# Optimization experiments

Hardware: AMD Instinct MI355X
Metric: run time of the kernel (lower is better)

## Reference

```python
import jax, jax.numpy as jnp
import numpy as np

LN_EPS = 1e-5

def _conv1d(x, w, b):
    # x: [B, T, Cin], w: [Cout, Cin, K] (torch layout), pad=1 -> same length for K=3
    y = jax.lax.conv_general_dilated(
        x, jnp.transpose(w, (2, 1, 0)), window_strides=(1,), padding=[(1, 1)],
        dimension_numbers=('NWC', 'WIO', 'NWC'))
    return y + b

def _layernorm(x, g, b):
    mu = jnp.mean(x, axis=-1, keepdims=True)
    var = jnp.mean(jnp.square(x - mu), axis=-1, keepdims=True)
    return (x - mu) * jax.lax.rsqrt(var + LN_EPS) * g + b

def _duration_predictor(enc, mask, w1, b1, g1, beta1, w2, b2, g2, beta2, wl, bl):
    x = enc * mask                                  # [B,T,C]
    x = _layernorm(jax.nn.relu(_conv1d(x, w1, b1)), g1, beta1)
    x = _layernorm(jax.nn.relu(_conv1d(x, w2, b2)), g2, beta2)
    out = x @ wl.T + bl                             # [B,T,1]
    return (out * mask)[..., 0]                     # [B,T]

def _expand_one(enc_i, dur_i, M):
    # enc_i: [T,C], dur_i: [T] int; fused repeat_interleave via searchsorted gather
    cs = jnp.cumsum(dur_i)                          # [T]
    pos = jnp.arange(M)                             # [M]
    idx = jnp.searchsorted(cs, pos, side='right')   # token index for each frame
    valid = pos < cs[-1]
    out = jnp.where(valid[:, None], enc_i[jnp.clip(idx, 0, enc_i.shape[0] - 1)], 0.0)
    dec = jnp.where(valid, pos + 1, 0)
    return out, dec

def setup_inputs() -> dict:
    key = jax.random.key(0)
    ks = jax.random.split(key, 12)
    B, T, C, F, M = 32, 512, 384, 384, 2048
    s = lambda n: 1.0 / np.sqrt(n)
    return {
        'encoder_output': jax.random.normal(ks[0], (B, T, C), jnp.float32),
        'encoder_output_mask': jnp.ones((B, T, 1), jnp.float32),
        'target': jax.random.randint(ks[1], (B, T), 0, 8, jnp.int32),
        'mel_max_length': M,
        'w1': jax.random.normal(ks[2], (F, C, 3), jnp.float32) * s(C * 3),
        'b1': jnp.zeros((F,), jnp.float32),
        'g1': jnp.ones((F,), jnp.float32),
        'beta1': jnp.zeros((F,), jnp.float32),
        'w2': jax.random.normal(ks[3], (F, F, 3), jnp.float32) * s(F * 3),
        'b2': jnp.zeros((F,), jnp.float32),
        'g2': jnp.ones((F,), jnp.float32),
        'beta2': jnp.zeros((F,), jnp.float32),
        'wl': jax.random.normal(ks[4], (1, F), jnp.float32) * s(F),
        'bl': jnp.zeros((1,), jnp.float32),
    }

def reference(encoder_output, encoder_output_mask, target, mel_max_length,
              w1, b1, g1, beta1, w2, b2, g2, beta2, wl, bl):
    # training-mode forward: durations come from `target`, alpha=1.0
    dpo = _duration_predictor(encoder_output, encoder_output_mask,
                              w1, b1, g1, beta1, w2, b2, g2, beta2, wl, bl)
    repeats = jnp.round(target.astype(jnp.float32) * 1.0).astype(jnp.int32)
    output, dec_pos = jax.vmap(lambda e, d: _expand_one(e, d, mel_max_length))(
        encoder_output, repeats)
    return output, dec_pos, dpo
```

## Files before the change

### kernel.cpp

```cpp
#include <hip/hip_runtime.h>
#include <hip/hip_bf16.h>
#include <stdint.h>

#define B_ 32
#define T_ 512
#define C_ 384
#define F_ 384
#define M_ 2048
#define PT (T_ + 2)
#define KTOT (3 * C_)

typedef __bf16 bf16x8 __attribute__((ext_vector_type(8)));
typedef float  f32x4  __attribute__((ext_vector_type(4)));
typedef unsigned short ushort_t;

__device__ __forceinline__ ushort_t f2bf(float f) {
  __hip_bfloat16 h = __float2bfloat16(f);
  return *reinterpret_cast<ushort_t*>(&h);
}
__device__ __forceinline__ uint32_t pack2(float a, float b) {
  return (uint32_t)f2bf(a) | ((uint32_t)f2bf(b) << 16);
}

#define NWB 3456
__global__ __launch_bounds__(256) void prep_kernel(
    const int* __restrict__ target,
    const float* __restrict__ w1, const float* __restrict__ w2,
    ushort_t* __restrict__ x1p,
    ushort_t* __restrict__ wt1, ushort_t* __restrict__ wt2,
    int* __restrict__ cs) {
  const int gid = blockIdx.x;
  const int tid = threadIdx.x;
  if (gid < NWB) {
    int idx = gid * 256 + tid;
    int w = idx >= F_ * KTOT;
    int o = idx - (w ? F_ * KTOT : 0);
    int n = o / KTOT, k = o - n * KTOT;
    int kk = k / C_, c = k - kk * C_;
    int s = kk * 6 + (c >> 6);
    int c64 = c & 63;
    int ks = c64 >> 5, qq = (c64 >> 3) & 3, e = c64 & 7;
    int wv = n / 48, rn = n - wv * 48, fn = rn >> 4, r16 = rn & 15;
    int lane = qq * 16 + r16;
    size_t dst = ((((size_t)s * 8 + wv) * 6 + fn * 2 + ks) << 9) + lane * 8 + e;
    const float* src = w ? w2 : w1;
    (w ? wt2 : wt1)[dst] = f2bf(src[(n * C_ + c) * 3 + kk]);
  } else if (gid < NWB + 48) {
    int idx = (gid - NWB) * 256 + tid;
    int bb = idx / C_, c = idx - bb * C_;
    x1p[(size_t)(bb * PT) * C_ + c] = 0;
    x1p[(size_t)(bb * PT + T_ + 1) * C_ + c] = 0;
  } else {
    int b = (gid - NWB - 48) * 4 + (tid >> 6);
    int lane = tid & 63;
    int base = b * T_ + lane * 8;
    int v[8];
#pragma unroll
    for (int i = 0; i < 8; ++i) v[i] = target[base + i];
#pragma unroll
    for (int i = 1; i < 8; ++i) v[i] += v[i - 1];
    int tot = v[7];
    int inc = tot;
#pragma unroll
    for (int d = 1; d < 64; d <<= 1) {
      int t = __shfl_up(inc, d);
      if (lane >= d) inc += t;
    }
    int excl = inc - tot;
#pragma unroll
    for (int i = 0; i < 8; ++i) cs[base + i] = v[i] + excl;
  }
}

template <bool LAST>
__global__ __launch_bounds__(512, 1) void gemm_ln_kernel(
    const float* __restrict__ enc,
    const float* __restrict__ mask,
    const ushort_t* __restrict__ x1p,
    const ushort_t* __restrict__ wt,
    const float* __restrict__ bias, const float* __restrict__ g,
    const float* __restrict__ be,
    const float* __restrict__ wl, const float* __restrict__ bl,
    ushort_t* __restrict__ xout,
    float* __restrict__ dpo) {
  __shared__ char ldsX[66 * 768];
  __shared__ float red[8][64][2];
  __shared__ float stats[64][2];

  const int tid = threadIdx.x;
  const int l = tid & 63, q = l >> 4, r16 = l & 15;
  const int wid = tid >> 6;
  const int b = blockIdx.x >> 3, t0 = (blockIdx.x & 7) * 64;

  if (!LAST) {
#pragma unroll
    for (int ps = 0; ps < 7; ++ps) {
      int idx = ps * 512 + tid;
      if (idx < 66 * 48) {
        int rl = idx / 48, cp = idx - rl * 48;
        int gc = cp >> 3, ch = cp & 7;
        int t = t0 - 1 + rl;
        uint4 o = make_uint4(0, 0, 0, 0);
        if (t >= 0 && t < T_) {
          const float* src = enc + ((size_t)b * T_ + t) * C_ + gc * 64 + ch * 8;
          float4 u = *(const float4*)src;
          float4 v = *(const float4*)(src + 4);
          float m = mask[b * T_ + t];
          o = make_uint4(pack2(u.x * m, u.y * m), pack2(u.z * m, u.w * m),
                         pack2(v.x * m, v.y * m), pack2(v.z * m, v.w * m));
        }
        *(uint4*)(ldsX + rl * 768 + gc * 128 + ((ch ^ (rl & 7)) << 4)) = o;
      }
    }
  } else {
#pragma unroll
    for (int ps = 0; ps < 7; ++ps) {
      int idx = ps * 512 + tid;
      if (idx < 66 * 48) {
        int rl = idx / 48, cp = idx - rl * 48;
        int gc = cp >> 3, ch = cp & 7;
        uint4 v = *(const uint4*)(x1p + ((size_t)(b * PT + t0 + rl)) * C_ +
                                  gc * 64 + ch * 8);
        *(uint4*)(ldsX + rl * 768 + gc * 128 + ((ch ^ (rl & 7)) << 4)) = v;
      }
    }
  }

  f32x4 acc[3][4];
#pragma unroll
  for (int fn = 0; fn < 3; ++fn)
#pragma unroll
    for (int fm = 0; fm < 4; ++fm) acc[fn][fm] = (f32x4){0.f, 0.f, 0.f, 0.f};

  const ushort_t* wlane = wt + ((size_t)wid * 6 << 9) + (l << 3);
  auto LOADW = [&](bf16x8 (&dst)[3][2], int s) {
    const ushort_t* p = wlane + (((size_t)s * 8 * 6) << 9);
#pragma unroll
    for (int fn = 0; fn < 3; ++fn)
#pragma unroll
      for (int ks = 0; ks < 2; ++ks)
        dst[fn][ks] = *(const bf16x8*)(p + ((fn * 2 + ks) << 9));
  };
  auto COMP = [&](bf16x8 (&af)[3][2], int s) {
    const int kk = s / 6, c128 = (s % 6) * 128;
#pragma unroll
    for (int ks = 0; ks < 2; ++ks) {
      bf16x8 bx[4];
#pragma unroll
      for (int fm = 0; fm < 4; ++fm) {
        int rl = fm * 16 + r16 + kk;
        bx[fm] = *(const bf16x8*)(ldsX + rl * 768 + c128 +
                                  (((ks * 4 + q) ^ (rl & 7)) << 4));
      }
#pragma unroll
      for (int fn = 0; fn < 3; ++fn)
#pragma unroll
        for (int fm = 0; fm < 4; ++fm)
          acc[fn][fm] = __builtin_amdgcn_mfma_f32_16x16x32_bf16(
              af[fn][ks], bx[fm], acc[fn][fm], 0, 0, 0);
    }
  };

  bf16x8 afA[3][2], afB[3][2];
  LOADW(afA, 0);
  __syncthreads();
#pragma unroll 1
  for (int s = 0; s < 18; s += 2) {
    LOADW(afB, s + 1);
    COMP(afA, s);
    if (s + 2 < 18) LOADW(afA, s + 2);
    COMP(afB, s + 1);
  }

#pragma unroll
  for (int fn = 0; fn < 3; ++fn) {
    const int nb = wid * 48 + fn * 16 + q * 4;
    float b0 = bias[nb], b1 = bias[nb + 1], b2 = bias[nb + 2], b3 = bias[nb + 3];
#pragma unroll
    for (int fm = 0; fm < 4; ++fm) {
      acc[fn][fm][0] = fmaxf(acc[fn][fm][0] + b0, 0.f);
      acc[fn][fm][1] = fmaxf(acc[fn][fm][1] + b1, 0.f);
      acc[fn][fm][2] = fmaxf(acc[fn][fm][2] + b2, 0.f);
      acc[fn][fm][3] = fmaxf(acc[fn][fm][3] + b3, 0.f);
    }
  }

#pragma unroll
  for (int fm = 0; fm < 4; ++fm) {
    float s = 0.f, s2 = 0.f;
#pragma unroll
    for (int fn = 0; fn < 3; ++fn)
#pragma unroll
      for (int j = 0; j < 4; ++j) {
        float v = acc[fn][fm][j];
        s += v; s2 += v * v;
      }
    s += __shfl_xor(s, 16); s += __shfl_xor(s, 32);
    s2 += __shfl_xor(s2, 16); s2 += __shfl_xor(s2, 32);
    if (l < 16) { red[wid][fm * 16 + r16][0] = s; red[wid][fm * 16 + r16][1] = s2; }
  }
  __syncthreads();
  if (tid < 64) {
    float S = 0.f, S2 = 0.f;
#pragma unroll
    for (int w = 0; w < 8; ++w) { S += red[w][tid][0]; S2 += red[w][tid][1]; }
    float mu = S / F_;
    stats[tid][0] = mu;
    stats[tid][1] = rsqrtf(S2 / F_ - mu * mu + 1e-5f);
  }
  __syncthreads();

  if (!LAST) {
#pragma unroll
    for (int fn = 0; fn < 3; ++fn) {
      const int nb = wid * 48 + fn * 16 + q * 4;
      float g0 = g[nb], g1 = g[nb + 1], g2 = g[nb + 2], g3 = g[nb + 3];
      float e0 = be[nb], e1 = be[nb + 1], e2 = be[nb + 2], e3 = be[nb + 3];
#pragma unroll
      for (int fm = 0; fm < 4; ++fm) {
        const int m = fm * 16 + r16;
        const float mu = stats[m][0], rs = stats[m][1];
        uint32_t p0 = pack2((acc[fn][fm][0] - mu) * rs * g0 + e0,
                            (acc[fn][fm][1] - mu) * rs * g1 + e1);
        uint32_t p1 = pack2((acc[fn][fm][2] - mu) * rs * g2 + e2,
                            (acc[fn][fm][3] - mu) * rs * g3 + e3);
        *(uint2*)(xout + ((size_t)(b * PT + 1 + t0 + m)) * C_ + nb) =
            make_uint2(p0, p1);
      }
    }
  } else {
    float p[4] = {0.f, 0.f, 0.f, 0.f};
#pragma unroll
    for (int fn = 0; fn < 3; ++fn) {
      const int nb = wid * 48 + fn * 16 + q * 4;
      float g0 = g[nb], g1 = g[nb + 1], g2 = g[nb + 2], g3 = g[nb + 3];
      float e0 = be[nb], e1 = be[nb + 1], e2 = be[nb + 2], e3 = be[nb + 3];
      float l0 = wl[nb], l1 = wl[nb + 1], l2 = wl[nb + 2], l3 = wl[nb + 3];
#pragma unroll
      for (int fm = 0; fm < 4; ++fm) {
        const int m = fm * 16 + r16;
        const float mu = stats[m][0], rs = stats[m][1];
        p[fm] += ((acc[fn][fm][0] - mu) * rs * g0 + e0) * l0 +
                 ((acc[fn][fm][1] - mu) * rs * g1 + e1) * l1 +
                 ((acc[fn][fm][2] - mu) * rs * g2 + e2) * l2 +
                 ((acc[fn][fm][3] - mu) * rs * g3 + e3) * l3;
      }
    }
    __syncthreads();
#pragma unroll
    for (int fm = 0; fm < 4; ++fm) {
      float s = p[fm];
      s += __shfl_xor(s, 16); s += __shfl_xor(s, 32);
      if (l < 16) red[wid][fm * 16 + r16][0] = s;
    }
    __syncthreads();
    if (tid < 64) {
      float S = 0.f;
#pragma unroll
      for (int w = 0; w < 8; ++w) S += red[w][tid][0];
      int t = t0 + tid;
      dpo[b * T_ + t] = (S + bl[0]) * mask[b * T_ + t];
    }
  }
}

__global__ __launch_bounds__(256) void expand_kernel(
    const float* __restrict__ enc,
    const int* __restrict__ cs,
    float* __restrict__ out,
    float* __restrict__ dec) {
  __shared__ int scs[T_];
  const int blk = blockIdx.x;
  const int b = blk / (M_ / 4);
  const int p0 = (blk - b * (M_ / 4)) * 4;
  for (int i = threadIdx.x; i < T_; i += 256) scs[i] = cs[b * T_ + i];
  __syncthreads();

  const int lane = threadIdx.x & 63;
  const int wid = threadIdx.x >> 6;
  const int pos = p0 + wid;
  const int total = scs[T_ - 1];
  const bool valid = pos < total;

  int idx = 0;
#pragma unroll
  for (int step = 512; step; step >>= 1)
    if (idx + step <= T_ && scs[idx + step - 1] <= pos) idx += step;
  int src = idx < T_ ? idx : T_ - 1;

  const float4* srow = (const float4*)(enc + ((size_t)b * T_ + src) * C_);
  float4* orow = (float4*)(out + ((size_t)b * M_ + pos) * C_);
  const float4 zero = make_float4(0.f, 0.f, 0.f, 0.f);
#pragma unroll
  for (int j = 0; j < 2; ++j) {
    int c4 = j * 64 + lane;
    if (c4 < C_ / 4) orow[c4] = valid ? srow[c4] : zero;
  }
  if (lane == 0) dec[b * M_ + pos] = valid ? (float)(pos + 1) : 0.f;
}

extern "C" void kernel_launch(void* const* d_in, const int* in_sizes, int n_in,
                              void* d_out, int out_size, void* d_ws,
                              size_t ws_size, hipStream_t stream) {
  const float* enc    = (const float*)d_in[0];
  const float* mask   = (const float*)d_in[1];
  const int*   target = (const int*)d_in[2];
  const float* w1    = (const float*)d_in[4];
  const float* b1    = (const float*)d_in[5];
  const float* g1    = (const float*)d_in[6];
  const float* beta1 = (const float*)d_in[7];
  const float* w2    = (const float*)d_in[8];
  const float* b2    = (const float*)d_in[9];
  const float* g2    = (const float*)d_in[10];
  const float* beta2 = (const float*)d_in[11];
  const float* wl    = (const float*)d_in[12];
  const float* bl    = (const float*)d_in[13];

  ushort_t* x1p = (ushort_t*)d_ws;
  ushort_t* wt1 = x1p + (size_t)B_ * PT * C_;
  ushort_t* wt2 = wt1 + (size_t)F_ * KTOT;
  int*      cs  = (int*)(wt2 + (size_t)F_ * KTOT);

  float* out0 = (float*)d_out;
  float* dec  = out0 + (size_t)B_ * M_ * C_;
  float* dpo  = dec + (size_t)B_ * M_;

  prep_kernel<<<NWB + 48 + 8, 256, 0, stream>>>(
      target, w1, w2, x1p, wt1, wt2, cs);

  gemm_ln_kernel<false><<<B_ * (T_ / 64), 512, 0, stream>>>(
      enc, mask, nullptr, wt1, b1, g1, beta1, nullptr, nullptr, x1p, nullptr);
  gemm_ln_kernel<true><<<B_ * (T_ / 64), 512, 0, stream>>>(
      nullptr, mask, x1p, wt2, b2, g2, beta2, wl, bl, nullptr, dpo);

  expand_kernel<<<(B_ * M_) / 4, 256, 0, stream>>>(enc, cs, out0, dec);
}
```

Before: 80.93 us.

## Fuse expand work into GEMM-LN launches as extra heterogeneous blocks

Drops the separate expand kernel and splits its gather-copy work into two halves, each handled by 256 extra blocks appended to the two conv GEMM+LayerNorm launches. The memory-bound expand copy can then run on CUs alongside the compute-bound GEMM blocks, which also removes one launch. Launch bounds are raised to two blocks per CU, and the weight double-buffer prefetch is restructured to load both stages inside each loop iteration. This lowers register pressure but weakens the overlap of weight loads with MFMA work.

New measurement: 111.5 us. +37.8%, slower.

```diff
diff --git a/kernel.cpp b/kernel.cpp
--- a/kernel.cpp
+++ b/kernel.cpp
@@ -72,17 +72,20 @@
   }
 }
 
-template <bool LAST>
-__global__ __launch_bounds__(512, 1) void gemm_ln_kernel(
+template <int PART>
+__global__ __launch_bounds__(512, 2) void hetero_kernel(
     const float* __restrict__ enc,
     const float* __restrict__ mask,
-    const ushort_t* __restrict__ x1p,
+    const ushort_t* __restrict__ x1p_in,
+    ushort_t* __restrict__ x1p_out,
     const ushort_t* __restrict__ wt,
     const float* __restrict__ bias, const float* __restrict__ g,
     const float* __restrict__ be,
     const float* __restrict__ wl, const float* __restrict__ bl,
-    ushort_t* __restrict__ xout,
-    float* __restrict__ dpo) {
+    float* __restrict__ dpo,
+    const int* __restrict__ cs,
+    float* __restrict__ out0,
+    float* __restrict__ dec) {
   __shared__ char ldsX[66 * 768];
   __shared__ float red[8][64][2];
   __shared__ float stats[64][2];
@@ -90,9 +93,37 @@
   const int tid = threadIdx.x;
   const int l = tid & 63, q = l >> 4, r16 = l & 15;
   const int wid = tid >> 6;
+
+  if (blockIdx.x >= 256) {
+    const int eb = blockIdx.x - 256;
+    const int b = eb >> 3;
+    const int p0 = (eb & 7) * 128 + PART * (M_ / 2);
+    int* scs = (int*)ldsX;
+    for (int i = tid; i < T_; i += 512) scs[i] = cs[b * T_ + i];
+    __syncthreads();
+    const int total = scs[T_ - 1];
+    const float4 zero = make_float4(0.f, 0.f, 0.f, 0.f);
+#pragma unroll 1
+    for (int it = 0; it < 16; ++it) {
+      const int pos = p0 + it * 8 + wid;
+      const bool valid = pos < total;
+      int idx = 0;
+#pragma unroll
+      for (int step = 512; step; step >>= 1)
+        if (idx + step <= T_ && scs[idx + step - 1] <= pos) idx += step;
+      int src = idx < T_ ? idx : T_ - 1;
+      const float4* srow = (const float4*)(enc + ((size_t)b * T_ + src) * C_);
+      float4* orow = (float4*)(out0 + ((size_t)b * M_ + pos) * C_);
+      orow[l] = valid ? srow[l] : zero;
+      if (l < 32) orow[64 + l] = valid ? srow[64 + l] : zero;
+      if (l == 0) dec[b * M_ + pos] = valid ? (float)(pos + 1) : 0.f;
+    }
+    return;
+  }
+
   const int b = blockIdx.x >> 3, t0 = (blockIdx.x & 7) * 64;
 
-  if (!LAST) {
+  if (PART == 0) {
 #pragma unroll
     for (int ps = 0; ps < 7; ++ps) {
       int idx = ps * 512 + tid;
@@ -119,7 +150,7 @@
       if (idx < 66 * 48) {
         int rl = idx / 48, cp = idx - rl * 48;
         int gc = cp >> 3, ch = cp & 7;
-        uint4 v = *(const uint4*)(x1p + ((size_t)(b * PT + t0 + rl)) * C_ +
+        uint4 v = *(const uint4*)(x1p_in + ((size_t)(b * PT + t0 + rl)) * C_ +
                                   gc * 64 + ch * 8);
         *(uint4*)(ldsX + rl * 768 + gc * 128 + ((ch ^ (rl & 7)) << 4)) = v;
       }
@@ -161,14 +192,13 @@
     }
   };
 
-  bf16x8 afA[3][2], afB[3][2];
-  LOADW(afA, 0);
   __syncthreads();
 #pragma unroll 1
   for (int s = 0; s < 18; s += 2) {
+    bf16x8 afA[3][2], afB[3][2];
+    LOADW(afA, s);
     LOADW(afB, s + 1);
     COMP(afA, s);
-    if (s + 2 < 18) LOADW(afA, s + 2);
     COMP(afB, s + 1);
   }
 
@@ -210,7 +240,7 @@
   }
   __syncthreads();
 
-  if (!LAST) {
+  if (PART == 0) {
 #pragma unroll
     for (int fn = 0; fn < 3; ++fn) {
       const int nb = wid * 48 + fn * 16 + q * 4;
@@ -224,7 +254,7 @@
                             (acc[fn][fm][1] - mu) * rs * g1 + e1);
         uint32_t p1 = pack2((acc[fn][fm][2] - mu) * rs * g2 + e2,
                             (acc[fn][fm][3] - mu) * rs * g3 + e3);
-        *(uint2*)(xout + ((size_t)(b * PT + 1 + t0 + m)) * C_ + nb) =
+        *(uint2*)(x1p_out + ((size_t)(b * PT + 1 + t0 + m)) * C_ + nb) =
             make_uint2(p0, p1);
       }
     }
@@ -262,41 +292,6 @@
       dpo[b * T_ + t] = (S + bl[0]) * mask[b * T_ + t];
     }
   }
-}
-
-__global__ __launch_bounds__(256) void expand_kernel(
-    const float* __restrict__ enc,
-    const int* __restrict__ cs,
-    float* __restrict__ out,
-    float* __restrict__ dec) {
-  __shared__ int scs[T_];
-  const int blk = blockIdx.x;
-  const int b = blk / (M_ / 4);
-  const int p0 = (blk - b * (M_ / 4)) * 4;
-  for (int i = threadIdx.x; i < T_; i += 256) scs[i] = cs[b * T_ + i];
-  __syncthreads();
-
-  const int lane = threadIdx.x & 63;
-  const int wid = threadIdx.x >> 6;
-  const int pos = p0 + wid;
-  const int total = scs[T_ - 1];
-  const bool valid = pos < total;
-
-  int idx = 0;
-#pragma unroll
-  for (int step = 512; step; step >>= 1)
-    if (idx + step <= T_ && scs[idx + step - 1] <= pos) idx += step;
-  int src = idx < T_ ? idx : T_ - 1;
-
-  const float4* srow = (const float4*)(enc + ((size_t)b * T_ + src) * C_);
-  float4* orow = (float4*)(out + ((size_t)b * M_ + pos) * C_);
-  const float4 zero = make_float4(0.f, 0.f, 0.f, 0.f);
-#pragma unroll
-  for (int j = 0; j < 2; ++j) {
-    int c4 = j * 64 + lane;
-    if (c4 < C_ / 4) orow[c4] = valid ? srow[c4] : zero;
-  }
-  if (lane == 0) dec[b * M_ + pos] = valid ? (float)(pos + 1) : 0.f;
 }
 
 extern "C" void kernel_launch(void* const* d_in, const int* in_sizes, int n_in,
@@ -328,10 +323,10 @@
   prep_kernel<<<NWB + 48 + 8, 256, 0, stream>>>(
       target, w1, w2, x1p, wt1, wt2, cs);
 
-  gemm_ln_kernel<false><<<B_ * (T_ / 64), 512, 0, stream>>>(
-      enc, mask, nullptr, wt1, b1, g1, beta1, nullptr, nullptr, x1p, nullptr);
-  gemm_ln_kernel<true><<<B_ * (T_ / 64), 512, 0, stream>>>(
-      nullptr, mask, x1p, wt2, b2, g2, beta2, wl, bl, nullptr, dpo);
-
-  expand_kernel<<<(B_ * M_) / 4, 256, 0, stream>>>(enc, cs, out0, dec);
-}
+  hetero_kernel<0><<<512, 512, 0, stream>>>(
+      enc, mask, nullptr, x1p, wt1, b1, g1, beta1, nullptr, nullptr,
+      nullptr, cs, out0, dec);
+  hetero_kernel<1><<<512, 512, 0, stream>>>(
+      enc, mask, x1p, nullptr, wt2, b2, g2, beta2, wl, bl,
+      dpo, cs, out0, dec);
+}
```

## Fuse both conv+LayerNorm stages into one kernel using halo recompute

Applied to the files above, without the earlier changes.

Merges the two conv-GEMM+LayerNorm kernels into a single kernel. Each block loads a 2-row halo of input, computes conv1 over 80 rows (66 used) and writes the normalized bf16 result into LDS, then runs conv2 directly from LDS. This removes the global round trip of the intermediate activation, the padding-zero pass in the prep kernel, and one launch. The cost is about 25% extra conv1 MFMA work from the halo recompute, more accumulator registers and a larger LDS footprint.

Result: faster. 75.97 us (-6.1%).

```diff
diff --git a/kernel.cpp b/kernel.cpp
--- a/kernel.cpp
+++ b/kernel.cpp
@@ -7,7 +7,6 @@
 #define C_ 384
 #define F_ 384
 #define M_ 2048
-#define PT (T_ + 2)
 #define KTOT (3 * C_)
 
 typedef __bf16 bf16x8 __attribute__((ext_vector_type(8)));
@@ -26,7 +25,6 @@
 __global__ __launch_bounds__(256) void prep_kernel(
     const int* __restrict__ target,
     const float* __restrict__ w1, const float* __restrict__ w2,
-    ushort_t* __restrict__ x1p,
     ushort_t* __restrict__ wt1, ushort_t* __restrict__ wt2,
     int* __restrict__ cs) {
   const int gid = blockIdx.x;
@@ -45,13 +43,8 @@
     size_t dst = ((((size_t)s * 8 + wv) * 6 + fn * 2 + ks) << 9) + lane * 8 + e;
     const float* src = w ? w2 : w1;
     (w ? wt2 : wt1)[dst] = f2bf(src[(n * C_ + c) * 3 + kk]);
-  } else if (gid < NWB + 48) {
-    int idx = (gid - NWB) * 256 + tid;
-    int bb = idx / C_, c = idx - bb * C_;
-    x1p[(size_t)(bb * PT) * C_ + c] = 0;
-    x1p[(size_t)(bb * PT + T_ + 1) * C_ + c] = 0;
   } else {
-    int b = (gid - NWB - 48) * 4 + (tid >> 6);
+    int b = (gid - NWB) * 4 + (tid >> 6);
     int lane = tid & 63;
     int base = b * T_ + lane * 8;
     int v[8];
@@ -72,76 +65,163 @@
   }
 }
 
-template <bool LAST>
-__global__ __launch_bounds__(512, 1) void gemm_ln_kernel(
+__global__ __launch_bounds__(512, 1) void gemm12_kernel(
     const float* __restrict__ enc,
     const float* __restrict__ mask,
-    const ushort_t* __restrict__ x1p,
-    const ushort_t* __restrict__ wt,
-    const float* __restrict__ bias, const float* __restrict__ g,
-    const float* __restrict__ be,
+    const ushort_t* __restrict__ wt1,
+    const ushort_t* __restrict__ wt2,
+    const float* __restrict__ b1, const float* __restrict__ g1,
+    const float* __restrict__ be1,
+    const float* __restrict__ b2, const float* __restrict__ g2,
+    const float* __restrict__ be2,
     const float* __restrict__ wl, const float* __restrict__ bl,
-    ushort_t* __restrict__ xout,
     float* __restrict__ dpo) {
-  __shared__ char ldsX[66 * 768];
-  __shared__ float red[8][64][2];
-  __shared__ float stats[64][2];
+  __shared__ char ldsX[82 * 768];
+  __shared__ float red[8][80][2];
+  __shared__ float stats[80][2];
 
   const int tid = threadIdx.x;
   const int l = tid & 63, q = l >> 4, r16 = l & 15;
   const int wid = tid >> 6;
   const int b = blockIdx.x >> 3, t0 = (blockIdx.x & 7) * 64;
 
-  if (!LAST) {
-#pragma unroll
-    for (int ps = 0; ps < 7; ++ps) {
-      int idx = ps * 512 + tid;
-      if (idx < 66 * 48) {
-        int rl = idx / 48, cp = idx - rl * 48;
-        int gc = cp >> 3, ch = cp & 7;
-        int t = t0 - 1 + rl;
-        uint4 o = make_uint4(0, 0, 0, 0);
-        if (t >= 0 && t < T_) {
-          const float* src = enc + ((size_t)b * T_ + t) * C_ + gc * 64 + ch * 8;
-          float4 u = *(const float4*)src;
-          float4 v = *(const float4*)(src + 4);
-          float m = mask[b * T_ + t];
-          o = make_uint4(pack2(u.x * m, u.y * m), pack2(u.z * m, u.w * m),
-                         pack2(v.x * m, v.y * m), pack2(v.z * m, v.w * m));
-        }
-        *(uint4*)(ldsX + rl * 768 + gc * 128 + ((ch ^ (rl & 7)) << 4)) = o;
-      }
-    }
-  } else {
-#pragma unroll
-    for (int ps = 0; ps < 7; ++ps) {
-      int idx = ps * 512 + tid;
-      if (idx < 66 * 48) {
-        int rl = idx / 48, cp = idx - rl * 48;
-        int gc = cp >> 3, ch = cp & 7;
-        uint4 v = *(const uint4*)(x1p + ((size_t)(b * PT + t0 + rl)) * C_ +
-                                  gc * 64 + ch * 8);
-        *(uint4*)(ldsX + rl * 768 + gc * 128 + ((ch ^ (rl & 7)) << 4)) = v;
-      }
-    }
-  }
-
-  f32x4 acc[3][4];
+#pragma unroll
+  for (int ps = 0; ps < 8; ++ps) {
+    int idx = ps * 512 + tid;
+    if (idx < 82 * 48) {
+      int rl = idx / 48, cp = idx - rl * 48;
+      int gc = cp >> 3, ch = cp & 7;
+      int t = t0 - 2 + rl;
+      uint4 o = make_uint4(0, 0, 0, 0);
+      if (t >= 0 && t < T_) {
+        const float* src = enc + ((size_t)b * T_ + t) * C_ + gc * 64 + ch * 8;
+        float4 u = *(const float4*)src;
+        float4 v = *(const float4*)(src + 4);
+        float m = mask[b * T_ + t];
+        o = make_uint4(pack2(u.x * m, u.y * m), pack2(u.z * m, u.w * m),
+                       pack2(v.x * m, v.y * m), pack2(v.z * m, v.w * m));
+      }
+      *(uint4*)(ldsX + rl * 768 + gc * 128 + ((ch ^ (rl & 7)) << 4)) = o;
+    }
+  }
+
+  f32x4 acc1[3][5];
 #pragma unroll
   for (int fn = 0; fn < 3; ++fn)
 #pragma unroll
-    for (int fm = 0; fm < 4; ++fm) acc[fn][fm] = (f32x4){0.f, 0.f, 0.f, 0.f};
-
-  const ushort_t* wlane = wt + ((size_t)wid * 6 << 9) + (l << 3);
-  auto LOADW = [&](bf16x8 (&dst)[3][2], int s) {
-    const ushort_t* p = wlane + (((size_t)s * 8 * 6) << 9);
+    for (int fm = 0; fm < 5; ++fm) acc1[fn][fm] = (f32x4){0.f, 0.f, 0.f, 0.f};
+
+  const ushort_t* wlane1 = wt1 + ((size_t)wid * 6 << 9) + (l << 3);
+  const ushort_t* wlane2 = wt2 + ((size_t)wid * 6 << 9) + (l << 3);
+  auto LOADW = [&](const ushort_t* wlane, bf16x8 (&dst)[3][2], int s) {
+    const ushort_t* p = wlane + (((size_t)s * 48) << 9);
 #pragma unroll
     for (int fn = 0; fn < 3; ++fn)
 #pragma unroll
       for (int ks = 0; ks < 2; ++ks)
         dst[fn][ks] = *(const bf16x8*)(p + ((fn * 2 + ks) << 9));
   };
-  auto COMP = [&](bf16x8 (&af)[3][2], int s) {
+  auto COMP1 = [&](bf16x8 (&af)[3][2], int s) {
+    const int kk = s / 6, c128 = (s % 6) * 128;
+#pragma unroll
+    for (int ks = 0; ks < 2; ++ks) {
+      bf16x8 bx[5];
+#pragma unroll
+      for (int fm = 0; fm < 5; ++fm) {
+        int rl = fm * 16 + r16 + kk;
+        bx[fm] = *(const bf16x8*)(ldsX + rl * 768 + c128 +
+                                  (((ks * 4 + q) ^ (rl & 7)) << 4));
+      }
+#pragma unroll
+      for (int fn = 0; fn < 3; ++fn)
+#pragma unroll
+        for (int fm = 0; fm < 5; ++fm)
+          acc1[fn][fm] = __builtin_amdgcn_mfma_f32_16x16x32_bf16(
+              af[fn][ks], bx[fm], acc1[fn][fm], 0, 0, 0);
+    }
+  };
+
+  {
+    bf16x8 afA[3][2], afB[3][2];
+    LOADW(wlane1, afA, 0);
+    __syncthreads();
+#pragma unroll 1
+    for (int s = 0; s < 18; s += 2) {
+      LOADW(wlane1, afB, s + 1);
+      COMP1(afA, s);
+      if (s + 2 < 18) LOADW(wlane1, afA, s + 2);
+      COMP1(afB, s + 1);
+    }
+  }
+
+#pragma unroll
+  for (int fn = 0; fn < 3; ++fn) {
+    const int nb = wid * 48 + fn * 16 + q * 4;
+    float c0 = b1[nb], c1 = b1[nb + 1], c2 = b1[nb + 2], c3 = b1[nb + 3];
+#pragma unroll
+    for (int fm = 0; fm < 5; ++fm) {
+      acc1[fn][fm][0] = fmaxf(acc1[fn][fm][0] + c0, 0.f);
+      acc1[fn][fm][1] = fmaxf(acc1[fn][fm][1] + c1, 0.f);
+      acc1[fn][fm][2] = fmaxf(acc1[fn][fm][2] + c2, 0.f);
+      acc1[fn][fm][3] = fmaxf(acc1[fn][fm][3] + c3, 0.f);
+    }
+  }
+#pragma unroll
+  for (int fm = 0; fm < 5; ++fm) {
+    float s = 0.f, s2 = 0.f;
+#pragma unroll
+    for (int fn = 0; fn < 3; ++fn)
+#pragma unroll
+      for (int j = 0; j < 4; ++j) {
+        float v = acc1[fn][fm][j];
+        s += v; s2 += v * v;
+      }
+    s += __shfl_xor(s, 16); s += __shfl_xor(s, 32);
+    s2 += __shfl_xor(s2, 16); s2 += __shfl_xor(s2, 32);
+    if (l < 16) { red[wid][fm * 16 + r16][0] = s; red[wid][fm * 16 + r16][1] = s2; }
+  }
+  __syncthreads();
+  if (tid < 66) {
+    float S = 0.f, S2 = 0.f;
+#pragma unroll
+    for (int w = 0; w < 8; ++w) { S += red[w][tid][0]; S2 += red[w][tid][1]; }
+    float mu = S / F_;
+    stats[tid][0] = mu;
+    stats[tid][1] = rsqrtf(S2 / F_ - mu * mu + 1e-5f);
+  }
+  __syncthreads();
+
+#pragma unroll
+  for (int fn = 0; fn < 3; ++fn) {
+    const int nb = wid * 48 + fn * 16 + q * 4;
+    float g0 = g1[nb], gg1 = g1[nb + 1], g2v = g1[nb + 2], g3 = g1[nb + 3];
+    float e0 = be1[nb], e1 = be1[nb + 1], e2 = be1[nb + 2], e3 = be1[nb + 3];
+#pragma unroll
+    for (int fm = 0; fm < 5; ++fm) {
+      const int m = fm * 16 + r16;
+      if (m < 66) {
+        const float mu = stats[m][0], rs = stats[m][1];
+        uint32_t p0 = pack2((acc1[fn][fm][0] - mu) * rs * g0 + e0,
+                            (acc1[fn][fm][1] - mu) * rs * gg1 + e1);
+        uint32_t p1 = pack2((acc1[fn][fm][2] - mu) * rs * g2v + e2,
+                            (acc1[fn][fm][3] - mu) * rs * g3 + e3);
+        *(uint2*)(ldsX + m * 768 + (((nb >> 3) ^ (m & 7)) << 4) +
+                  ((q & 1) << 3)) = make_uint2(p0, p1);
+      }
+    }
+  }
+  if (t0 == 0 && tid < 48)
+    *(uint4*)(ldsX + tid * 16) = make_uint4(0, 0, 0, 0);
+  if (t0 == T_ - 64 && tid < 48)
+    *(uint4*)(ldsX + 65 * 768 + tid * 16) = make_uint4(0, 0, 0, 0);
+
+  f32x4 acc2[3][4];
+#pragma unroll
+  for (int fn = 0; fn < 3; ++fn)
+#pragma unroll
+    for (int fm = 0; fm < 4; ++fm) acc2[fn][fm] = (f32x4){0.f, 0.f, 0.f, 0.f};
+
+  auto COMP2 = [&](bf16x8 (&af)[3][2], int s) {
     const int kk = s / 6, c128 = (s % 6) * 128;
 #pragma unroll
     for (int ks = 0; ks < 2; ++ks) {
@@ -156,35 +236,37 @@
       for (int fn = 0; fn < 3; ++fn)
 #pragma unroll
         for (int fm = 0; fm < 4; ++fm)
-          acc[fn][fm] = __builtin_amdgcn_mfma_f32_16x16x32_bf16(
-              af[fn][ks], bx[fm], acc[fn][fm], 0, 0, 0);
+          acc2[fn][fm] = __builtin_amdgcn_mfma_f32_16x16x32_bf16(
+              af[fn][ks], bx[fm], acc2[fn][fm], 0, 0, 0);
     }
   };
 
-  bf16x8 afA[3][2], afB[3][2];
-  LOADW(afA, 0);
-  __syncthreads();
+  {
+    bf16x8 afA[3][2], afB[3][2];
+    LOADW(wlane2, afA, 0);
+    __syncthreads();
 #pragma unroll 1
-  for (int s = 0; s < 18; s += 2) {
-    LOADW(afB, s + 1);
-    COMP(afA, s);
-    if (s + 2 < 18) LOADW(afA, s + 2);
-    COMP(afB, s + 1);
+    for (int s = 0; s < 18; s += 2) {
+      LOADW(wlane2, afB, s + 1);
+      COMP2(afA, s);
+      if (s + 2 < 18) LOADW(wlane2, afA, s + 2);
+      COMP2(afB, s + 1);
+    }
   }
 
 #pragma unroll
   for (int fn = 0; fn < 3; ++fn) {
     const int nb = wid * 48 + fn * 16 + q * 4;
-    float b0 = bias[nb], b1 = bias[nb + 1], b2 = bias[nb + 2], b3 = bias[nb + 3];
+    float c0 = b2[nb], c1 = b2[nb + 1], c2 = b2[nb + 2], c3 = b2[nb + 3];
 #pragma unroll
     for (int fm = 0; fm < 4; ++fm) {
-      acc[fn][fm][0] = fmaxf(acc[fn][fm][0] + b0, 0.f);
-      acc[fn][fm][1] = fmaxf(acc[fn][fm][1] + b1, 0.f);
-      acc[fn][fm][2] = fmaxf(acc[fn][fm][2] + b2, 0.f);
-      acc[fn][fm][3] = fmaxf(acc[fn][fm][3] + b3, 0.f);
-    }
-  }
-
+      acc2[fn][fm][0] = fmaxf(acc2[fn][fm][0] + c0, 0.f);
+      acc2[fn][fm][1] = fmaxf(acc2[fn][fm][1] + c1, 0.f);
+      acc2[fn][fm][2] = fmaxf(acc2[fn][fm][2] + c2, 0.f);
+      acc2[fn][fm][3] = fmaxf(acc2[fn][fm][3] + c3, 0.f);
+    }
+  }
+  __syncthreads();
 #pragma unroll
   for (int fm = 0; fm < 4; ++fm) {
     float s = 0.f, s2 = 0.f;
@@ -192,7 +274,7 @@
     for (int fn = 0; fn < 3; ++fn)
 #pragma unroll
       for (int j = 0; j < 4; ++j) {
-        float v = acc[fn][fm][j];
+        float v = acc2[fn][fm][j];
         s += v; s2 += v * v;
       }
     s += __shfl_xor(s, 16); s += __shfl_xor(s, 32);
@@ -210,57 +292,37 @@
   }
   __syncthreads();
 
-  if (!LAST) {
-#pragma unroll
-    for (int fn = 0; fn < 3; ++fn) {
-      const int nb = wid * 48 + fn * 16 + q * 4;
-      float g0 = g[nb], g1 = g[nb + 1], g2 = g[nb + 2], g3 = g[nb + 3];
-      float e0 = be[nb], e1 = be[nb + 1], e2 = be[nb + 2], e3 = be[nb + 3];
-#pragma unroll
-      for (int fm = 0; fm < 4; ++fm) {
-        const int m = fm * 16 + r16;
-        const float mu = stats[m][0], rs = stats[m][1];
-        uint32_t p0 = pack2((acc[fn][fm][0] - mu) * rs * g0 + e0,
-                            (acc[fn][fm][1] - mu) * rs * g1 + e1);
-        uint32_t p1 = pack2((acc[fn][fm][2] - mu) * rs * g2 + e2,
-                            (acc[fn][fm][3] - mu) * rs * g3 + e3);
-        *(uint2*)(xout + ((size_t)(b * PT + 1 + t0 + m)) * C_ + nb) =
-            make_uint2(p0, p1);
-      }
-    }
-  } else {
-    float p[4] = {0.f, 0.f, 0.f, 0.f};
-#pragma unroll
-    for (int fn = 0; fn < 3; ++fn) {
-      const int nb = wid * 48 + fn * 16 + q * 4;
-      float g0 = g[nb], g1 = g[nb + 1], g2 = g[nb + 2], g3 = g[nb + 3];
-      float e0 = be[nb], e1 = be[nb + 1], e2 = be[nb + 2], e3 = be[nb + 3];
-      float l0 = wl[nb], l1 = wl[nb + 1], l2 = wl[nb + 2], l3 = wl[nb + 3];
-#pragma unroll
-      for (int fm = 0; fm < 4; ++fm) {
-        const int m = fm * 16 + r16;
-        const float mu = stats[m][0], rs = stats[m][1];
-        p[fm] += ((acc[fn][fm][0] - mu) * rs * g0 + e0) * l0 +
-                 ((acc[fn][fm][1] - mu) * rs * g1 + e1) * l1 +
-                 ((acc[fn][fm][2] - mu) * rs * g2 + e2) * l2 +
-                 ((acc[fn][fm][3] - mu) * rs * g3 + e3) * l3;
-      }
-    }
-    __syncthreads();
+  float p[4] = {0.f, 0.f, 0.f, 0.f};
+#pragma unroll
+  for (int fn = 0; fn < 3; ++fn) {
+    const int nb = wid * 48 + fn * 16 + q * 4;
+    float g0 = g2[nb], gg1 = g2[nb + 1], g2v = g2[nb + 2], g3 = g2[nb + 3];
+    float e0 = be2[nb], e1 = be2[nb + 1], e2 = be2[nb + 2], e3 = be2[nb + 3];
+    float l0 = wl[nb], l1 = wl[nb + 1], l2 = wl[nb + 2], l3 = wl[nb + 3];
 #pragma unroll
     for (int fm = 0; fm < 4; ++fm) {
-      float s = p[fm];
-      s += __shfl_xor(s, 16); s += __shfl_xor(s, 32);
-      if (l < 16) red[wid][fm * 16 + r16][0] = s;
-    }
-    __syncthreads();
-    if (tid < 64) {
-      float S = 0.f;
-#pragma unroll
-      for (int w = 0; w < 8; ++w) S += red[w][tid][0];
-      int t = t0 + tid;
-      dpo[b * T_ + t] = (S + bl[0]) * mask[b * T_ + t];
-    }
+      const int m = fm * 16 + r16;
+      const float mu = stats[m][0], rs = stats[m][1];
+      p[fm] += ((acc2[fn][fm][0] - mu) * rs * g0 + e0) * l0 +
+               ((acc2[fn][fm][1] - mu) * rs * gg1 + e1) * l1 +
+               ((acc2[fn][fm][2] - mu) * rs * g2v + e2) * l2 +
+               ((acc2[fn][fm][3] - mu) * rs * g3 + e3) * l3;
+    }
+  }
+  __syncthreads();
+#pragma unroll
+  for (int fm = 0; fm < 4; ++fm) {
+    float s = p[fm];
+    s += __shfl_xor(s, 16); s += __shfl_xor(s, 32);
+    if (l < 16) red[wid][fm * 16 + r16][0] = s;
+  }
+  __syncthreads();
+  if (tid < 64) {
+    float S = 0.f;
+#pragma unroll
+    for (int w = 0; w < 8; ++w) S += red[w][tid][0];
+    int t = t0 + tid;
+    dpo[b * T_ + t] = (S + bl[0]) * mask[b * T_ + t];
   }
 }
 
@@ -316,8 +378,7 @@
   const float* wl    = (const float*)d_in[12];
   const float* bl    = (const float*)d_in[13];
 
-  ushort_t* x1p = (ushort_t*)d_ws;
-  ushort_t* wt1 = x1p + (size_t)B_ * PT * C_;
+  ushort_t* wt1 = (ushort_t*)d_ws;
   ushort_t* wt2 = wt1 + (size_t)F_ * KTOT;
   int*      cs  = (int*)(wt2 + (size_t)F_ * KTOT);
 
@@ -325,13 +386,10 @@
   float* dec  = out0 + (size_t)B_ * M_ * C_;
   float* dpo  = dec + (size_t)B_ * M_;
 
-  prep_kernel<<<NWB + 48 + 8, 256, 0, stream>>>(
-      target, w1, w2, x1p, wt1, wt2, cs);
-
-  gemm_ln_kernel<false><<<B_ * (T_ / 64), 512, 0, stream>>>(
-      enc, mask, nullptr, wt1, b1, g1, beta1, nullptr, nullptr, x1p, nullptr);
-  gemm_ln_kernel<true><<<B_ * (T_ / 64), 512, 0, stream>>>(
-      nullptr, mask, x1p, wt2, b2, g2, beta2, wl, bl, nullptr, dpo);
+  prep_kernel<<<NWB + 8, 256, 0, stream>>>(target, w1, w2, wt1, wt2, cs);
+
+  gemm12_kernel<<<256, 512, 0, stream>>>(
+      enc, mask, wt1, wt2, b1, g1, beta1, b2, g2, beta2, wl, bl, dpo);
 
   expand_kernel<<<(B_ * M_) / 4, 256, 0, stream>>>(enc, cs, out0, dec);
 }
```

## Fuse expand into prep kernel and compute per-block cumsum in LDS

Applied to the files above, without the earlier changes.

The separate expand kernel is removed and its work moves into the prep kernel as extra blocks. Each expand block recomputes the per-batch cumulative sum of durations directly into shared memory instead of reading a global cs buffer, and each block now handles 16 frame positions instead of 4. This removes one kernel launch and the global cs round trip. In exchange, the prefix scan is repeated once per block, and the expand work now runs before the GEMM kernels rather than after.

Measured after the change: 69.64 us. 1.16x faster.

```diff
diff --git a/kernel.cpp b/kernel.cpp
--- a/kernel.cpp
+++ b/kernel.cpp
@@ -23,12 +23,16 @@
 }
 
 #define NWB 3456
-__global__ __launch_bounds__(256) void prep_kernel(
+#define NHB 48
+#define NEXB 4096
+__global__ __launch_bounds__(256) void prep_expand_kernel(
     const int* __restrict__ target,
     const float* __restrict__ w1, const float* __restrict__ w2,
+    const float* __restrict__ enc,
     ushort_t* __restrict__ x1p,
     ushort_t* __restrict__ wt1, ushort_t* __restrict__ wt2,
-    int* __restrict__ cs) {
+    float* __restrict__ out0,
+    float* __restrict__ dec) {
   const int gid = blockIdx.x;
   const int tid = threadIdx.x;
   if (gid < NWB) {
@@ -45,14 +49,22 @@
     size_t dst = ((((size_t)s * 8 + wv) * 6 + fn * 2 + ks) << 9) + lane * 8 + e;
     const float* src = w ? w2 : w1;
     (w ? wt2 : wt1)[dst] = f2bf(src[(n * C_ + c) * 3 + kk]);
-  } else if (gid < NWB + 48) {
+    return;
+  }
+  if (gid < NWB + NHB) {
     int idx = (gid - NWB) * 256 + tid;
     int bb = idx / C_, c = idx - bb * C_;
     x1p[(size_t)(bb * PT) * C_ + c] = 0;
     x1p[(size_t)(bb * PT + T_ + 1) * C_ + c] = 0;
-  } else {
-    int b = (gid - NWB - 48) * 4 + (tid >> 6);
-    int lane = tid & 63;
+    return;
+  }
+
+  __shared__ int scs[T_];
+  const int eb = gid - NWB - NHB;
+  const int b = eb >> 7;
+  const int p0 = (eb & 127) * 16;
+  if (tid < 64) {
+    int lane = tid;
     int base = b * T_ + lane * 8;
     int v[8];
 #pragma unroll
@@ -68,7 +80,27 @@
     }
     int excl = inc - tot;
 #pragma unroll
-    for (int i = 0; i < 8; ++i) cs[base + i] = v[i] + excl;
+    for (int i = 0; i < 8; ++i) scs[lane * 8 + i] = v[i] + excl;
+  }
+  __syncthreads();
+
+  const int lane = tid & 63, wid = tid >> 6;
+  const int total = scs[T_ - 1];
+  const float4 zero = make_float4(0.f, 0.f, 0.f, 0.f);
+#pragma unroll
+  for (int it = 0; it < 4; ++it) {
+    const int pos = p0 + it * 4 + wid;
+    const bool valid = pos < total;
+    int idx = 0;
+#pragma unroll
+    for (int step = 512; step; step >>= 1)
+      if (idx + step <= T_ && scs[idx + step - 1] <= pos) idx += step;
+    int src = idx < T_ ? idx : T_ - 1;
+    const float4* srow = (const float4*)(enc + ((size_t)b * T_ + src) * C_);
+    float4* orow = (float4*)(out0 + ((size_t)b * M_ + pos) * C_);
+    orow[lane] = valid ? srow[lane] : zero;
+    if (lane < 32) orow[64 + lane] = valid ? srow[64 + lane] : zero;
+    if (lane == 0) dec[b * M_ + pos] = valid ? (float)(pos + 1) : 0.f;
   }
 }
 
@@ -264,41 +296,6 @@
   }
 }
 
-__global__ __launch_bounds__(256) void expand_kernel(
-    const float* __restrict__ enc,
-    const int* __restrict__ cs,
-    float* __restrict__ out,
-    float* __restrict__ dec) {
-  __shared__ int scs[T_];
-  const int blk = blockIdx.x;
-  const int b = blk / (M_ / 4);
-  const int p0 = (blk - b * (M_ / 4)) * 4;
-  for (int i = threadIdx.x; i < T_; i += 256) scs[i] = cs[b * T_ + i];
-  __syncthreads();
-
-  const int lane = threadIdx.x & 63;
-  const int wid = threadIdx.x >> 6;
-  const int pos = p0 + wid;
-  const int total = scs[T_ - 1];
-  const bool valid = pos < total;
-
-  int idx = 0;
-#pragma unroll
-  for (int step = 512; step; step >>= 1)
-    if (idx + step <= T_ && scs[idx + step - 1] <= pos) idx += step;
-  int src = idx < T_ ? idx : T_ - 1;
-
-  const float4* srow = (const float4*)(enc + ((size_t)b * T_ + src) * C_);
-  float4* orow = (float4*)(out + ((size_t)b * M_ + pos) * C_);
-  const float4 zero = make_float4(0.f, 0.f, 0.f, 0.f);
-#pragma unroll
-  for (int j = 0; j < 2; ++j) {
-    int c4 = j * 64 + lane;
-    if (c4 < C_ / 4) orow[c4] = valid ? srow[c4] : zero;
-  }
-  if (lane == 0) dec[b * M_ + pos] = valid ? (float)(pos + 1) : 0.f;
-}
-
 extern "C" void kernel_launch(void* const* d_in, const int* in_sizes, int n_in,
                               void* d_out, int out_size, void* d_ws,
                               size_t ws_size, hipStream_t stream) {
@@ -319,19 +316,16 @@
   ushort_t* x1p = (ushort_t*)d_ws;
   ushort_t* wt1 = x1p + (size_t)B_ * PT * C_;
   ushort_t* wt2 = wt1 + (size_t)F_ * KTOT;
-  int*      cs  = (int*)(wt2 + (size_t)F_ * KTOT);
 
   float* out0 = (float*)d_out;
   float* dec  = out0 + (size_t)B_ * M_ * C_;
   float* dpo  = dec + (size_t)B_ * M_;
 
-  prep_kernel<<<NWB + 48 + 8, 256, 0, stream>>>(
-      target, w1, w2, x1p, wt1, wt2, cs);
+  prep_expand_kernel<<<NWB + NHB + NEXB, 256, 0, stream>>>(
+      target, w1, w2, enc, x1p, wt1, wt2, out0, dec);
 
   gemm_ln_kernel<false><<<B_ * (T_ / 64), 512, 0, stream>>>(
       enc, mask, nullptr, wt1, b1, g1, beta1, nullptr, nullptr, x1p, nullptr);
   gemm_ln_kernel<true><<<B_ * (T_ / 64), 512, 0, stream>>>(
       nullptr, mask, x1p, wt2, b2, g2, beta2, wl, bl, nullptr, dpo);
-
-  expand_kernel<<<(B_ * M_) / 4, 256, 0, stream>>>(enc, cs, out0, dec);
-}
+}
```
